# Optimization experiments

Measured on AMD Instinct MI355X. Metric: run time of the kernel, lower is better.

Reference implementation:

```python
import jax, jax.numpy as jnp
import numpy as np

B, H, W, C = 32, 112, 112, 128
R = 2048  # make_divisible(128*16, 8)

def setup_inputs() -> dict:
    key = jax.random.key(0)
    k1, k2, k3 = jax.random.split(key, 3)
    x = jax.random.normal(k1, (B, H, W, C), dtype=jnp.float32)
    w1 = jax.random.normal(k2, (C, R), dtype=jnp.float32) * (1.0 / np.sqrt(C))
    b1 = jnp.zeros((R,), dtype=jnp.float32)
    w2 = jax.random.normal(k3, (R, C), dtype=jnp.float32) * (1.0 / np.sqrt(R))
    b2 = jnp.zeros((C,), dtype=jnp.float32)
    return {"x": x, "w1": w1, "b1": b1, "w2": w2, "b2": b2}

def reference(x, w1, b1, w2, b2):
    # squeeze: global average pool over H, W -> [B, C]
    s = jnp.mean(x, axis=(1, 2))
    # excite: two 1x1 convs on pooled vector == matmuls
    h = jax.nn.gelu(s @ w1 + b1)          # [B, R], tanh-approx GELU (tfa default)
    g = jax.nn.sigmoid(h @ w2 + b2)       # [B, C]
    # broadcast gate over spatial dims
    return x * g[:, None, None, :]
```

## Files before the change

kernel.cpp:

```cpp
#include <hip/hip_runtime.h>
#include <math.h>

#define B_ 32
#define H_ 112
#define W_ 112
#define C_ 128
#define R_ 2048
#define HW_ (H_ * W_)
#define C4_ (C_ / 4)
#define POOL_BLOCKS_PER_B 16

__global__ __launch_bounds__(256) void pool_kernel(const float4* __restrict__ x,
                                                   float* __restrict__ s) {
    const int b     = blockIdx.x;
    const int pb    = blockIdx.y;
    const int t     = threadIdx.x;
    const int lane4 = t & 31;
    const int prow  = t >> 5;

    const int pixels_per_block = HW_ / POOL_BLOCKS_PER_B;
    const int p0 = pb * pixels_per_block;
    const float4* xb = x + (size_t)b * HW_ * C4_;

    float4 acc = make_float4(0.f, 0.f, 0.f, 0.f);
    for (int p = p0 + prow; p < p0 + pixels_per_block; p += 8) {
        float4 v = xb[(size_t)p * C4_ + lane4];
        acc.x += v.x; acc.y += v.y; acc.z += v.z; acc.w += v.w;
    }

    __shared__ float4 red[256];
    red[t] = acc;
    __syncthreads();
    if (t < 32) {
        float4 a = red[t];
#pragma unroll
        for (int k = 1; k < 8; ++k) {
            float4 v = red[t + 32 * k];
            a.x += v.x; a.y += v.y; a.z += v.z; a.w += v.w;
        }
        float* sb = s + b * C_ + t * 4;
        atomicAdd(sb + 0, a.x);
        atomicAdd(sb + 1, a.y);
        atomicAdd(sb + 2, a.z);
        atomicAdd(sb + 3, a.w);
    }
}

__global__ __launch_bounds__(256) void fc1_kernel(const float* __restrict__ s,
                                                  const float* __restrict__ w1,
                                                  const float* __restrict__ b1,
                                                  float* __restrict__ h) {
    const int b  = blockIdx.x >> 3;
    const int rb = blockIdx.x & 7;
    const int r  = rb * 256 + threadIdx.x;

    __shared__ float sl[C_];
    if (threadIdx.x < C_)
        sl[threadIdx.x] = s[b * C_ + threadIdx.x] * (1.0f / (float)HW_);
    __syncthreads();

    float acc = b1[r];
#pragma unroll 8
    for (int c = 0; c < C_; ++c)
        acc += sl[c] * w1[(size_t)c * R_ + r];

    const float xv = acc;
    const float tn = tanhf(0.7978845608028654f * (xv + 0.044715f * xv * xv * xv));
    h[(size_t)b * R_ + r] = 0.5f * xv * (1.0f + tn);
}

__global__ __launch_bounds__(256) void fc2_kernel(const float* __restrict__ h,
                                                  const float* __restrict__ w2,
                                                  const float* __restrict__ b2,
                                                  float* __restrict__ g) {
    const int b    = blockIdx.x;
    const int t    = threadIdx.x;
    const int c    = t & 127;
    const int half = t >> 7;

    __shared__ float hl[R_];
    for (int i = t; i < R_; i += 256) hl[i] = h[(size_t)b * R_ + i];
    __syncthreads();

    float acc = 0.f;
    const int r0 = half * (R_ / 2);
#pragma unroll 8
    for (int r = r0; r < r0 + R_ / 2; ++r)
        acc += hl[r] * w2[(size_t)r * C_ + c];

    __shared__ float part[256];
    part[t] = acc;
    __syncthreads();
    if (t < 128) {
        const float v = part[t] + part[t + 128] + b2[t];
        g[b * C_ + t] = 1.0f / (1.0f + expf(-v));
    }
}

__global__ __launch_bounds__(256) void scale_kernel(const float4* __restrict__ x,
                                                    const float4* __restrict__ g,
                                                    float4* __restrict__ out) {
    const int b  = blockIdx.x;
    const int t  = threadIdx.x;
    const int c4 = t & 31;

    const float4 gv = g[b * C4_ + c4];
    const size_t base = (size_t)b * HW_ * C4_;
    const int total = HW_ * C4_;
    const int stride = gridDim.y * 256;

    for (int i = blockIdx.y * 256 + t; i < total; i += stride) {
        float4 v = x[base + i];
        v.x *= gv.x; v.y *= gv.y; v.z *= gv.z; v.w *= gv.w;
        out[base + i] = v;
    }
}

extern "C" void kernel_launch(void* const* d_in, const int* in_sizes, int n_in,
                              void* d_out, int out_size, void* d_ws, size_t ws_size,
                              hipStream_t stream) {
    const float* x  = (const float*)d_in[0];
    const float* w1 = (const float*)d_in[1];
    const float* b1 = (const float*)d_in[2];
    const float* w2 = (const float*)d_in[3];
    const float* b2 = (const float*)d_in[4];
    float* out = (float*)d_out;

    float* s = (float*)d_ws;
    float* h = s + B_ * C_;
    float* g = h + B_ * R_;

    hipMemsetAsync(s, 0, B_ * C_ * sizeof(float), stream);

    pool_kernel<<<dim3(B_, POOL_BLOCKS_PER_B), 256, 0, stream>>>((const float4*)x, s);
    fc1_kernel<<<B_ * 8, 256, 0, stream>>>(s, w1, b1, h);
    fc2_kernel<<<B_, 256, 0, stream>>>(h, w2, b2, g);
    scale_kernel<<<dim3(B_, 64), 256, 0, stream>>>((const float4*)x, (const float4*)g,
                                                   (float4*)out);
}
```

Measured before the change: 469.0 us.

## Replace pool atomics with partial sums, vectorize fc2, nontemporal output stores

The pool kernel now writes per-block partial sums to a workspace buffer instead of using atomics. This removes the memset launch, and the pool grid doubles to 32 blocks per batch. fc1 reduces those partials itself. fc2 is restructured to read w2 as float4 over 8 row slices, with a shared-memory reduction. The scale kernel uses nontemporal stores so the large output does not pollute cache, though it may lose L2 reuse of x between pool and scale.

```diff
diff --git a/kernel.cpp b/kernel.cpp
--- a/kernel.cpp
+++ b/kernel.cpp
@@ -8,17 +8,19 @@
 #define R_ 2048
 #define HW_ (H_ * W_)
 #define C4_ (C_ / 4)
-#define POOL_BLOCKS_PER_B 16
+#define PB_ 32
+
+typedef float f32x4_t __attribute__((ext_vector_type(4)));
 
 __global__ __launch_bounds__(256) void pool_kernel(const float4* __restrict__ x,
-                                                   float* __restrict__ s) {
+                                                   float4* __restrict__ part) {
     const int b     = blockIdx.x;
     const int pb    = blockIdx.y;
     const int t     = threadIdx.x;
     const int lane4 = t & 31;
     const int prow  = t >> 5;
 
-    const int pixels_per_block = HW_ / POOL_BLOCKS_PER_B;
+    const int pixels_per_block = HW_ / PB_;
     const int p0 = pb * pixels_per_block;
     const float4* xb = x + (size_t)b * HW_ * C4_;
 
@@ -38,25 +40,33 @@
             float4 v = red[t + 32 * k];
             a.x += v.x; a.y += v.y; a.z += v.z; a.w += v.w;
         }
-        float* sb = s + b * C_ + t * 4;
-        atomicAdd(sb + 0, a.x);
-        atomicAdd(sb + 1, a.y);
-        atomicAdd(sb + 2, a.z);
-        atomicAdd(sb + 3, a.w);
+        part[((size_t)b * PB_ + pb) * C4_ + t] = a;
     }
 }
 
-__global__ __launch_bounds__(256) void fc1_kernel(const float* __restrict__ s,
+__global__ __launch_bounds__(256) void fc1_kernel(const float4* __restrict__ part,
                                                   const float* __restrict__ w1,
                                                   const float* __restrict__ b1,
                                                   float* __restrict__ h) {
     const int b  = blockIdx.x >> 3;
     const int rb = blockIdx.x & 7;
     const int r  = rb * 256 + threadIdx.x;
+    const int t  = threadIdx.x;
 
     __shared__ float sl[C_];
-    if (threadIdx.x < C_)
-        sl[threadIdx.x] = s[b * C_ + threadIdx.x] * (1.0f / (float)HW_);
+    if (t < 32) {
+        float4 a = make_float4(0.f, 0.f, 0.f, 0.f);
+#pragma unroll 8
+        for (int k = 0; k < PB_; ++k) {
+            float4 v = part[((size_t)b * PB_ + k) * C4_ + t];
+            a.x += v.x; a.y += v.y; a.z += v.z; a.w += v.w;
+        }
+        const float inv = 1.0f / (float)HW_;
+        sl[t * 4 + 0] = a.x * inv;
+        sl[t * 4 + 1] = a.y * inv;
+        sl[t * 4 + 2] = a.z * inv;
+        sl[t * 4 + 3] = a.w * inv;
+    }
     __syncthreads();
 
     float acc = b1[r];
@@ -70,30 +80,45 @@
 }
 
 __global__ __launch_bounds__(256) void fc2_kernel(const float* __restrict__ h,
-                                                  const float* __restrict__ w2,
+                                                  const float4* __restrict__ w2,
                                                   const float* __restrict__ b2,
-                                                  float* __restrict__ g) {
-    const int b    = blockIdx.x;
-    const int t    = threadIdx.x;
-    const int c    = t & 127;
-    const int half = t >> 7;
+                                                  float4* __restrict__ g) {
+    const int b     = blockIdx.x;
+    const int t     = threadIdx.x;
+    const int c4    = t & 31;
+    const int slice = t >> 5;
 
     __shared__ float hl[R_];
     for (int i = t; i < R_; i += 256) hl[i] = h[(size_t)b * R_ + i];
     __syncthreads();
 
-    float acc = 0.f;
-    const int r0 = half * (R_ / 2);
-#pragma unroll 8
-    for (int r = r0; r < r0 + R_ / 2; ++r)
-        acc += hl[r] * w2[(size_t)r * C_ + c];
+    float4 acc = make_float4(0.f, 0.f, 0.f, 0.f);
+    const int r0 = slice * (R_ / 8);
+#pragma unroll 4
+    for (int r = r0; r < r0 + R_ / 8; ++r) {
+        const float hv = hl[r];
+        float4 w = w2[(size_t)r * C4_ + c4];
+        acc.x += hv * w.x; acc.y += hv * w.y; acc.z += hv * w.z; acc.w += hv * w.w;
+    }
 
-    __shared__ float part[256];
-    part[t] = acc;
+    __shared__ float4 partl[256];
+    partl[t] = acc;
     __syncthreads();
-    if (t < 128) {
-        const float v = part[t] + part[t + 128] + b2[t];
-        g[b * C_ + t] = 1.0f / (1.0f + expf(-v));
+    if (t < 32) {
+        float4 a = partl[t];
+#pragma unroll
+        for (int k = 1; k < 8; ++k) {
+            float4 v = partl[t + 32 * k];
+            a.x += v.x; a.y += v.y; a.z += v.z; a.w += v.w;
+        }
+        a.x += b2[t * 4 + 0]; a.y += b2[t * 4 + 1];
+        a.z += b2[t * 4 + 2]; a.w += b2[t * 4 + 3];
+        float4 gv;
+        gv.x = 1.0f / (1.0f + expf(-a.x));
+        gv.y = 1.0f / (1.0f + expf(-a.y));
+        gv.z = 1.0f / (1.0f + expf(-a.z));
+        gv.w = 1.0f / (1.0f + expf(-a.w));
+        g[(size_t)b * C4_ + t] = gv;
     }
 }
 
@@ -104,15 +129,16 @@
     const int t  = threadIdx.x;
     const int c4 = t & 31;
 
-    const float4 gv = g[b * C4_ + c4];
+    const float4 gv = g[(size_t)b * C4_ + c4];
     const size_t base = (size_t)b * HW_ * C4_;
     const int total = HW_ * C4_;
     const int stride = gridDim.y * 256;
 
     for (int i = blockIdx.y * 256 + t; i < total; i += stride) {
         float4 v = x[base + i];
-        v.x *= gv.x; v.y *= gv.y; v.z *= gv.z; v.w *= gv.w;
-        out[base + i] = v;
+        f32x4_t o;
+        o.x = v.x * gv.x; o.y = v.y * gv.y; o.z = v.z * gv.z; o.w = v.w * gv.w;
+        __builtin_nontemporal_store(o, (f32x4_t*)&out[base + i]);
     }
 }
 
@@ -126,15 +152,13 @@
     const float* b2 = (const float*)d_in[4];
     float* out = (float*)d_out;
 
-    float* s = (float*)d_ws;
-    float* h = s + B_ * C_;
-    float* g = h + B_ * R_;
+    float* part = (float*)d_ws;
+    float* h    = part + B_ * PB_ * C_;
+    float* g    = h + B_ * R_;
 
-    hipMemsetAsync(s, 0, B_ * C_ * sizeof(float), stream);
-
-    pool_kernel<<<dim3(B_, POOL_BLOCKS_PER_B), 256, 0, stream>>>((const float4*)x, s);
-    fc1_kernel<<<B_ * 8, 256, 0, stream>>>(s, w1, b1, h);
-    fc2_kernel<<<B_, 256, 0, stream>>>(h, w2, b2, g);
+    pool_kernel<<<dim3(B_, PB_), 256, 0, stream>>>((const float4*)x, (float4*)part);
+    fc1_kernel<<<B_ * 8, 256, 0, stream>>>((const float4*)part, w1, b1, h);
+    fc2_kernel<<<B_, 256, 0, stream>>>(h, (const float4*)w2, b2, (float4*)g);
     scale_kernel<<<dim3(B_, 64), 256, 0, stream>>>((const float4*)x, (const float4*)g,
                                                    (float4*)out);
 }
```

Result: faster. 422.2 us (-10.0%).
